# Kernel tuning notes

Measured on AMD Instinct MI355X. Metric: run time of the kernel, lower is better.

Reference implementation:

```python
import jax, jax.numpy as jnp
import numpy as np

B, N, D = 4, 2048, 512
H, HD = 8, 64  # heads, output_dim per head


def setup_inputs() -> dict:
    key = jax.random.key(0)
    ks = jax.random.split(key, 6)
    x = jax.random.normal(ks[0], (B, N, D), dtype=jnp.float32)
    adj = (jax.random.uniform(ks[1], (N, N)) < 0.1).astype(jnp.float32)
    adj = jnp.maximum(adj, jnp.eye(N, dtype=jnp.float32))
    s = 0.02
    Wq = jax.random.normal(ks[2], (D, H * HD), dtype=jnp.float32) * s
    Wk = jax.random.normal(ks[3], (D, H * HD), dtype=jnp.float32) * s
    Wv = jax.random.normal(ks[4], (D, H * HD), dtype=jnp.float32) * s
    bq = jnp.zeros((H * HD,), dtype=jnp.float32)
    bk = jnp.zeros((H * HD,), dtype=jnp.float32)
    bv = jnp.zeros((H * HD,), dtype=jnp.float32)
    return {"x": x, "adj": adj, "Wq": Wq, "bq": bq, "Wk": Wk, "bk": bk, "Wv": Wv, "bv": bv}


def reference(x, adj, Wq, bq, Wk, bk, Wv, bv):
    b, n, _ = x.shape
    q = (x @ Wq + bq).reshape(b, n, H, HD)
    k = (x @ Wk + bk).reshape(b, n, H, HD)
    v = (x @ Wv + bv).reshape(b, n, H, HD)
    # scores: [b, h, i, j]
    scores = jnp.einsum('bihd,bjhd->bhij', q, k) / jnp.sqrt(jnp.float32(HD))
    mask = jnp.where(adj == 0, jnp.float32(-1e9), jnp.float32(0.0))  # [n, n]
    scores = scores + mask[None, None, :, :]
    weights = jax.nn.softmax(scores, axis=-1)
    # dropout is identity at inference (training=False)
    out = jnp.einsum('bhij,bjhd->bihd', weights, v)
    return out.reshape(b, n, H * HD)
```

## Files before the change

### kernel.cpp

```cpp
#include <hip/hip_runtime.h>
#include <hip/hip_bf16.h>
#include <stdint.h>

#define NTOK 2048
#define DIN  512
#define QSCALE 0.18033688011112042f

typedef __attribute__((ext_vector_type(8))) short bf16x8;
typedef __attribute__((ext_vector_type(4))) short bf16x4;
typedef __attribute__((ext_vector_type(4))) float f32x4;

#define MFMA16(a, b, c) __builtin_amdgcn_mfma_f32_16x16x32_bf16((a), (b), (c), 0, 0, 0)

union u4bf8 { uint4 u; bf16x8 h; };

static __device__ __forceinline__ short f2bf(float f) {
  union { float f; uint32_t u; } v; v.f = f;
  uint32_t r = (v.u + 0x7FFFu + ((v.u >> 16) & 1u)) >> 16;
  return (short)r;
}

__global__ __launch_bounds__(256) void k_xbf(const float* __restrict__ x, short* __restrict__ xb) {
  size_t i = (size_t)blockIdx.x * 256 + threadIdx.x;
  const float4 v = *(const float4*)(x + i * 4);
  bf16x4 h;
  h[0] = f2bf(v.x); h[1] = f2bf(v.y); h[2] = f2bf(v.z); h[3] = f2bf(v.w);
  *(bf16x4*)(xb + i * 4) = h;
}

__global__ __launch_bounds__(256) void k_wt(const float* __restrict__ Wq,
                                            const float* __restrict__ Wk,
                                            const float* __restrict__ Wv,
                                            short* __restrict__ Wt) {
  const float* W = (blockIdx.z == 0) ? Wq : ((blockIdx.z == 1) ? Wk : Wv);
  short* Wo = Wt + (size_t)blockIdx.z * DIN * DIN;
  __shared__ float tile[32][33];
  int bo = blockIdx.x * 32, bc = blockIdx.y * 32;
  int tx = threadIdx.x & 31, ty = threadIdx.x >> 5;
#pragma unroll
  for (int q = 0; q < 4; ++q)
    tile[ty + q * 8][tx] = W[(bc + ty + q * 8) * DIN + bo + tx];
  __syncthreads();
#pragma unroll
  for (int q = 0; q < 4; ++q)
    Wo[(bo + ty + q * 8) * DIN + bc + tx] = f2bf(tile[tx][ty + q * 8]);
}

__global__ __launch_bounds__(256) void k_mask(const float* __restrict__ adj,
                                              unsigned long long* __restrict__ m64) {
  int wid = ((blockIdx.x * blockDim.x + threadIdx.x) >> 6);
  int lane = threadIdx.x & 63;
  int i = wid >> 5, wd = wid & 31;
  float a = adj[i * NTOK + wd * 64 + lane];
  unsigned long long b = __ballot(a != 0.0f);
  if (lane == 0) m64[i * 32 + wd] = b;
}

__global__ __launch_bounds__(256, 3) void k_qkv(const short* __restrict__ xb,
                                                const short* __restrict__ Wt,
                                                const float* __restrict__ bq,
                                                const float* __restrict__ bk,
                                                const float* __restrict__ bv,
                                                short* __restrict__ Qb, short* __restrict__ Kb,
                                                short* __restrict__ Vb) {
  __shared__ short As[2][128 * 40];
  __shared__ short Bs[2][128 * 40];
  const int z = blockIdx.z;
  const short* Wz = Wt + z * DIN * DIN;
  const float* bias = (z == 0) ? bq : ((z == 1) ? bk : bv);
  const int mbase = blockIdx.x * 128, nbase = blockIdx.y * 128;
  const int tid = threadIdx.x;
  const int lane = tid & 63, w = tid >> 6;
  const int wr = w >> 1, wc = w & 1;
  const int lrow = lane & 15, lgrp = lane >> 4;
  const int ra = tid >> 2, ca = tid & 3;

  f32x4 acc[4][4];
#pragma unroll
  for (int a = 0; a < 4; ++a)
#pragma unroll
    for (int b = 0; b < 4; ++b) acc[a][b] = (f32x4){0.f, 0.f, 0.f, 0.f};

  uint4 pA[2], pB[2];
#pragma unroll
  for (int u = 0; u < 2; ++u) {
    pA[u] = *(const uint4*)(xb + (size_t)(mbase + ra + u * 64) * DIN + ca * 8);
    pB[u] = *(const uint4*)(Wz + (size_t)(nbase + ra + u * 64) * DIN + ca * 8);
  }
#pragma unroll
  for (int u = 0; u < 2; ++u) {
    *(uint4*)(&As[0][(ra + u * 64) * 40 + ca * 8]) = pA[u];
    *(uint4*)(&Bs[0][(ra + u * 64) * 40 + ca * 8]) = pB[u];
  }
  __syncthreads();

  for (int t = 0; t < 16; ++t) {
    const int cur = t & 1, nxt = cur ^ 1;
    if (t < 15) {
      const int kb = (t + 1) * 32;
#pragma unroll
      for (int u = 0; u < 2; ++u) {
        pA[u] = *(const uint4*)(xb + (size_t)(mbase + ra + u * 64) * DIN + kb + ca * 8);
        pB[u] = *(const uint4*)(Wz + (size_t)(nbase + ra + u * 64) * DIN + kb + ca * 8);
      }
    }
    bf16x8 af[4], bf[4];
#pragma unroll
    for (int mi = 0; mi < 4; ++mi)
      af[mi] = *(bf16x8*)(&As[cur][(wr * 64 + mi * 16 + lrow) * 40 + lgrp * 8]);
#pragma unroll
    for (int ni = 0; ni < 4; ++ni)
      bf[ni] = *(bf16x8*)(&Bs[cur][(wc * 64 + ni * 16 + lrow) * 40 + lgrp * 8]);
#pragma unroll
    for (int mi = 0; mi < 4; ++mi)
#pragma unroll
      for (int ni = 0; ni < 4; ++ni) acc[mi][ni] = MFMA16(af[mi], bf[ni], acc[mi][ni]);

    if (t < 15) {
#pragma unroll
      for (int u = 0; u < 2; ++u) {
        *(uint4*)(&As[nxt][(ra + u * 64) * 40 + ca * 8]) = pA[u];
        *(uint4*)(&Bs[nxt][(ra + u * 64) * 40 + ca * 8]) = pB[u];
      }
      __syncthreads();
    }
  }

#pragma unroll
  for (int ni = 0; ni < 4; ++ni) {
    int go = nbase + wc * 64 + ni * 16 + lrow;
    float bv_ = bias[go];
    int h = go >> 6, d = go & 63;
#pragma unroll
    for (int mi = 0; mi < 4; ++mi) {
#pragma unroll
      for (int v = 0; v < 4; ++v) {
        int gm = mbase + wr * 64 + mi * 16 + lgrp * 4 + v;
        int b = gm >> 11, n = gm & 2047;
        int bh = b * 8 + h;
        float val = acc[mi][ni][v] + bv_;
        if (z == 0)
          Qb[(size_t)bh * (NTOK * 64) + n * 64 + d] = f2bf(val * QSCALE);
        else if (z == 1)
          Kb[(size_t)bh * (NTOK * 64) + n * 64 + d] = f2bf(val);
        else
          Vb[(size_t)bh * (64 * NTOK) + d * NTOK + n] = f2bf(val);
      }
    }
  }
}

__global__ __launch_bounds__(256, 3) void k_attn(const short* __restrict__ Qb,
                                                 const short* __restrict__ Kb,
                                                 const short* __restrict__ Vb,
                                                 const unsigned long long* __restrict__ m64,
                                                 float* __restrict__ out) {
  __shared__ char smem[36864];
  f32x4* ored = (f32x4*)smem;
  float* lsum = (float*)(smem + 16384);

  const int itile = blockIdx.x, bh = blockIdx.y;
  const int ibase = itile * 64;
  const int tid = threadIdx.x, lane = tid & 63, w = tid >> 6;
  const int wi = w >> 1, wj = w & 1;
  const int lrow = lane & 15, lgrp = lane >> 4;

  const short* Qp = Qb + (size_t)bh * (NTOK * 64);
  const short* Kp = Kb + (size_t)bh * (NTOK * 64);
  const short* Vp = Vb + (size_t)bh * (64 * NTOK);

  bf16x8 qa[2][2];
  const unsigned long long* mword[2];
#pragma unroll
  for (int ig = 0; ig < 2; ++ig) {
    const int qrow = ibase + wi * 32 + ig * 16 + lrow;
    qa[ig][0] = *(const bf16x8*)(Qp + (size_t)qrow * 64 + lgrp * 8);
    qa[ig][1] = *(const bf16x8*)(Qp + (size_t)qrow * 64 + 32 + lgrp * 8);
    mword[ig] = m64 + (size_t)qrow * 32;
  }

  const int r0 = tid >> 3, s0 = tid & 7;

  f32x4 oacc[2][4];
#pragma unroll
  for (int ig = 0; ig < 2; ++ig)
#pragma unroll
    for (int dn = 0; dn < 4; ++dn) oacc[ig][dn] = (f32x4){0.f, 0.f, 0.f, 0.f};
  float lrun[2] = {0.f, 0.f};

  uint4 pfK0 = *(const uint4*)(Kp + (size_t)r0 * 64 + s0 * 8);
  uint4 pfK1 = *(const uint4*)(Kp + (size_t)(r0 + 32) * 64 + s0 * 8);
  uint4 pfV0 = *(const uint4*)(Vp + (size_t)r0 * NTOK + s0 * 8);
  uint4 pfV1 = *(const uint4*)(Vp + (size_t)(r0 + 32) * NTOK + s0 * 8);
  unsigned long long mw[2] = {mword[0][0], mword[1][0]};
  {
    short* Kl0 = (short*)smem;
    short* Vl0 = (short*)(smem + 9216);
    *(uint4*)(Kl0 + r0 * 72 + s0 * 8) = pfK0;
    *(uint4*)(Kl0 + (r0 + 32) * 72 + s0 * 8) = pfK1;
    *(uint4*)(Vl0 + r0 * 72 + s0 * 8) = pfV0;
    *(uint4*)(Vl0 + (r0 + 32) * 72 + s0 * 8) = pfV1;
  }
  __syncthreads();

  for (int jt = 0; jt < 32; ++jt) {
    short* KlC = (short*)(smem + (jt & 1) * 18432);
    short* VlC = (short*)(smem + (jt & 1) * 18432 + 9216);
    unsigned long long mwn[2] = {0ull, 0ull};
    if (jt < 31) {
      const int jn = (jt + 1) * 64;
      pfK0 = *(const uint4*)(Kp + (size_t)(jn + r0) * 64 + s0 * 8);
      pfK1 = *(const uint4*)(Kp + (size_t)(jn + r0 + 32) * 64 + s0 * 8);
      pfV0 = *(const uint4*)(Vp + (size_t)r0 * NTOK + jn + s0 * 8);
      pfV1 = *(const uint4*)(Vp + (size_t)(r0 + 32) * NTOK + jn + s0 * 8);
      mwn[0] = mword[0][jt + 1];
      mwn[1] = mword[1][jt + 1];
    }

    uint32_t pk[2][2][2];
#pragma unroll
    for (int jsub = 0; jsub < 2; ++jsub) {
      const int krow = (wj * 32 + jsub * 16 + lrow) * 72;
      bf16x8 kf0 = *(bf16x8*)(KlC + krow + lgrp * 8);
      bf16x8 kf1 = *(bf16x8*)(KlC + krow + 32 + lgrp * 8);
#pragma unroll
      for (int ig = 0; ig < 2; ++ig) {
        f32x4 zz = (f32x4){0.f, 0.f, 0.f, 0.f};
        zz = MFMA16(kf0, qa[ig][0], zz);
        zz = MFMA16(kf1, qa[ig][1], zz);
        const uint32_t bits = (uint32_t)(mw[ig] >> (wj * 32 + jsub * 16 + lgrp * 4));
        float p0 = (bits & 1u) ? exp2f(zz[0]) : 0.f;
        float p1 = (bits & 2u) ? exp2f(zz[1]) : 0.f;
        float p2 = (bits & 4u) ? exp2f(zz[2]) : 0.f;
        float p3 = (bits & 8u) ? exp2f(zz[3]) : 0.f;
        lrun[ig] += (p0 + p1) + (p2 + p3);
        uint32_t w0, w1;
        asm("v_cvt_pk_bf16_f32 %0, %1, %2" : "=v"(w0) : "v"(p0), "v"(p1));
        asm("v_cvt_pk_bf16_f32 %0, %1, %2" : "=v"(w1) : "v"(p2), "v"(p3));
        pk[ig][jsub][0] = w0;
        pk[ig][jsub][1] = w1;
      }
    }

#pragma unroll
    for (int dn = 0; dn < 4; ++dn) {
      const int vrow = (dn * 16 + lrow) * 72 + wj * 32 + lgrp * 4;
      const uint2 v0 = *(const uint2*)(VlC + vrow);
      const uint2 v1 = *(const uint2*)(VlC + vrow + 16);
      u4bf8 vb;
      vb.u = (uint4){v0.x, v0.y, v1.x, v1.y};
#pragma unroll
      for (int ig = 0; ig < 2; ++ig) {
        u4bf8 pa;
        pa.u = (uint4){pk[ig][0][0], pk[ig][0][1], pk[ig][1][0], pk[ig][1][1]};
        oacc[ig][dn] = MFMA16(pa.h, vb.h, oacc[ig][dn]);
      }
    }

    if (jt < 31) {
      short* KlN = (short*)(smem + ((jt + 1) & 1) * 18432);
      short* VlN = (short*)(smem + ((jt + 1) & 1) * 18432 + 9216);
      *(uint4*)(KlN + r0 * 72 + s0 * 8) = pfK0;
      *(uint4*)(KlN + (r0 + 32) * 72 + s0 * 8) = pfK1;
      *(uint4*)(VlN + r0 * 72 + s0 * 8) = pfV0;
      *(uint4*)(VlN + (r0 + 32) * 72 + s0 * 8) = pfV1;
      mw[0] = mwn[0];
      mw[1] = mwn[1];
      __syncthreads();
    }
  }

  __syncthreads();

#pragma unroll
  for (int ig = 0; ig < 2; ++ig) {
    float s = lrun[ig];
    s += __shfl_xor(s, 16);
    s += __shfl_xor(s, 32);
    if (lane < 16) lsum[(w * 2 + ig) * 16 + lane] = s;
  }
  if (wj == 1) {
#pragma unroll
    for (int ig = 0; ig < 2; ++ig)
#pragma unroll
      for (int dn = 0; dn < 4; ++dn)
        ored[((wi * 2 + ig) * 4 + dn) * 64 + lane] = oacc[ig][dn];
  }
  __syncthreads();

  if (wj == 0) {
    const int b = bh >> 3, h = bh & 7;
#pragma unroll
    for (int ig = 0; ig < 2; ++ig) {
      const f32x4 la = *(const f32x4*)&lsum[((wi * 2 + 0) * 2 + ig) * 16 + lgrp * 4];
      const f32x4 lb = *(const f32x4*)&lsum[((wi * 2 + 1) * 2 + ig) * 16 + lgrp * 4];
      float inv[4];
#pragma unroll
      for (int v = 0; v < 4; ++v) inv[v] = 1.0f / (la[v] + lb[v]);
#pragma unroll
      for (int dn = 0; dn < 4; ++dn) {
        f32x4 s = oacc[ig][dn] + ored[((wi * 2 + ig) * 4 + dn) * 64 + lane];
#pragma unroll
        for (int v = 0; v < 4; ++v) {
          int i = ibase + wi * 32 + ig * 16 + lgrp * 4 + v;
          out[(size_t)(b * NTOK + i) * DIN + h * 64 + dn * 16 + lrow] = s[v] * inv[v];
        }
      }
    }
  }
}

extern "C" void kernel_launch(void* const* d_in, const int* in_sizes, int n_in,
                              void* d_out, int out_size, void* d_ws, size_t ws_size,
                              hipStream_t stream) {
  const float* x   = (const float*)d_in[0];
  const float* adj = (const float*)d_in[1];
  const float* Wq  = (const float*)d_in[2];
  const float* bq  = (const float*)d_in[3];
  const float* Wk  = (const float*)d_in[4];
  const float* bk  = (const float*)d_in[5];
  const float* Wv  = (const float*)d_in[6];
  const float* bv  = (const float*)d_in[7];
  float* out = (float*)d_out;

  char* ws = (char*)d_ws;
  short* Qb = (short*)(ws);
  short* Kb = (short*)(ws + (8u << 20));
  short* Vb = (short*)(ws + (16u << 20));
  short* Wt = (short*)(ws + (24u << 20));
  unsigned long long* m64 = (unsigned long long*)(ws + (26u << 20));
  short* xb = (short*)d_out;

  k_xbf<<<4096, 256, 0, stream>>>(x, xb);
  k_wt<<<dim3(16, 16, 3), 256, 0, stream>>>(Wq, Wk, Wv, Wt);
  k_mask<<<16384, 256, 0, stream>>>(adj, m64);
  k_qkv<<<dim3(64, 4, 3), 256, 0, stream>>>(xb, Wt, bq, bk, bv, Qb, Kb, Vb);
  k_attn<<<dim3(32, 32), 256, 0, stream>>>(Qb, Kb, Vb, m64, out);
}
```

Before: 120.7 us.

## Halve attention query tile to 32 rows and single-buffer K/V LDS

The attention kernel now processes 32 query rows per block instead of 64, doubling the grid to 64x32 blocks. K/V staging drops from double-buffered to single-buffered LDS, adding an extra barrier before each store, and launch bounds rise to 4 blocks per CU. The aim is higher occupancy and fewer per-thread registers, giving more blocks to fill the CUs. In exchange, each K/V tile is loaded from global memory twice as often, the extra barrier serialises load and compute, and MFMA work per LDS read is halved.

```diff
diff --git a/kernel.cpp b/kernel.cpp
--- a/kernel.cpp
+++ b/kernel.cpp
@@ -150,17 +150,19 @@
   }
 }
 
-__global__ __launch_bounds__(256, 3) void k_attn(const short* __restrict__ Qb,
+__global__ __launch_bounds__(256, 4) void k_attn(const short* __restrict__ Qb,
                                                  const short* __restrict__ Kb,
                                                  const short* __restrict__ Vb,
                                                  const unsigned long long* __restrict__ m64,
                                                  float* __restrict__ out) {
-  __shared__ char smem[36864];
+  __shared__ char smem[18432];
+  short* Kl = (short*)smem;
+  short* Vl = (short*)(smem + 9216);
   f32x4* ored = (f32x4*)smem;
-  float* lsum = (float*)(smem + 16384);
+  float* lsum = (float*)(smem + 8192);
 
   const int itile = blockIdx.x, bh = blockIdx.y;
-  const int ibase = itile * 64;
+  const int ibase = itile * 32;
   const int tid = threadIdx.x, lane = tid & 63, w = tid >> 6;
   const int wi = w >> 1, wj = w & 1;
   const int lrow = lane & 15, lgrp = lane >> 4;
@@ -169,142 +171,114 @@
   const short* Kp = Kb + (size_t)bh * (NTOK * 64);
   const short* Vp = Vb + (size_t)bh * (64 * NTOK);
 
-  bf16x8 qa[2][2];
-  const unsigned long long* mword[2];
-#pragma unroll
-  for (int ig = 0; ig < 2; ++ig) {
-    const int qrow = ibase + wi * 32 + ig * 16 + lrow;
-    qa[ig][0] = *(const bf16x8*)(Qp + (size_t)qrow * 64 + lgrp * 8);
-    qa[ig][1] = *(const bf16x8*)(Qp + (size_t)qrow * 64 + 32 + lgrp * 8);
-    mword[ig] = m64 + (size_t)qrow * 32;
-  }
+  const int qrow = ibase + wi * 16 + lrow;
+  bf16x8 qa[2];
+  qa[0] = *(const bf16x8*)(Qp + (size_t)qrow * 64 + lgrp * 8);
+  qa[1] = *(const bf16x8*)(Qp + (size_t)qrow * 64 + 32 + lgrp * 8);
+  const unsigned long long* mword = m64 + (size_t)qrow * 32;
 
   const int r0 = tid >> 3, s0 = tid & 7;
 
-  f32x4 oacc[2][4];
-#pragma unroll
-  for (int ig = 0; ig < 2; ++ig)
-#pragma unroll
-    for (int dn = 0; dn < 4; ++dn) oacc[ig][dn] = (f32x4){0.f, 0.f, 0.f, 0.f};
-  float lrun[2] = {0.f, 0.f};
+  f32x4 oacc[4];
+#pragma unroll
+  for (int dn = 0; dn < 4; ++dn) oacc[dn] = (f32x4){0.f, 0.f, 0.f, 0.f};
+  float lrun = 0.f;
 
   uint4 pfK0 = *(const uint4*)(Kp + (size_t)r0 * 64 + s0 * 8);
   uint4 pfK1 = *(const uint4*)(Kp + (size_t)(r0 + 32) * 64 + s0 * 8);
   uint4 pfV0 = *(const uint4*)(Vp + (size_t)r0 * NTOK + s0 * 8);
   uint4 pfV1 = *(const uint4*)(Vp + (size_t)(r0 + 32) * NTOK + s0 * 8);
-  unsigned long long mw[2] = {mword[0][0], mword[1][0]};
-  {
-    short* Kl0 = (short*)smem;
-    short* Vl0 = (short*)(smem + 9216);
-    *(uint4*)(Kl0 + r0 * 72 + s0 * 8) = pfK0;
-    *(uint4*)(Kl0 + (r0 + 32) * 72 + s0 * 8) = pfK1;
-    *(uint4*)(Vl0 + r0 * 72 + s0 * 8) = pfV0;
-    *(uint4*)(Vl0 + (r0 + 32) * 72 + s0 * 8) = pfV1;
-  }
+  unsigned long long mw = mword[0];
+  *(uint4*)(Kl + r0 * 72 + s0 * 8) = pfK0;
+  *(uint4*)(Kl + (r0 + 32) * 72 + s0 * 8) = pfK1;
+  *(uint4*)(Vl + r0 * 72 + s0 * 8) = pfV0;
+  *(uint4*)(Vl + (r0 + 32) * 72 + s0 * 8) = pfV1;
   __syncthreads();
 
   for (int jt = 0; jt < 32; ++jt) {
-    short* KlC = (short*)(smem + (jt & 1) * 18432);
-    short* VlC = (short*)(smem + (jt & 1) * 18432 + 9216);
-    unsigned long long mwn[2] = {0ull, 0ull};
+    unsigned long long mwn = 0ull;
     if (jt < 31) {
       const int jn = (jt + 1) * 64;
       pfK0 = *(const uint4*)(Kp + (size_t)(jn + r0) * 64 + s0 * 8);
       pfK1 = *(const uint4*)(Kp + (size_t)(jn + r0 + 32) * 64 + s0 * 8);
       pfV0 = *(const uint4*)(Vp + (size_t)r0 * NTOK + jn + s0 * 8);
       pfV1 = *(const uint4*)(Vp + (size_t)(r0 + 32) * NTOK + jn + s0 * 8);
-      mwn[0] = mword[0][jt + 1];
-      mwn[1] = mword[1][jt + 1];
-    }
-
-    uint32_t pk[2][2][2];
+      mwn = mword[jt + 1];
+    }
+
+    uint32_t pk[2][2];
 #pragma unroll
     for (int jsub = 0; jsub < 2; ++jsub) {
       const int krow = (wj * 32 + jsub * 16 + lrow) * 72;
-      bf16x8 kf0 = *(bf16x8*)(KlC + krow + lgrp * 8);
-      bf16x8 kf1 = *(bf16x8*)(KlC + krow + 32 + lgrp * 8);
-#pragma unroll
-      for (int ig = 0; ig < 2; ++ig) {
-        f32x4 zz = (f32x4){0.f, 0.f, 0.f, 0.f};
-        zz = MFMA16(kf0, qa[ig][0], zz);
-        zz = MFMA16(kf1, qa[ig][1], zz);
-        const uint32_t bits = (uint32_t)(mw[ig] >> (wj * 32 + jsub * 16 + lgrp * 4));
-        float p0 = (bits & 1u) ? exp2f(zz[0]) : 0.f;
-        float p1 = (bits & 2u) ? exp2f(zz[1]) : 0.f;
-        float p2 = (bits & 4u) ? exp2f(zz[2]) : 0.f;
-        float p3 = (bits & 8u) ? exp2f(zz[3]) : 0.f;
-        lrun[ig] += (p0 + p1) + (p2 + p3);
-        uint32_t w0, w1;
-        asm("v_cvt_pk_bf16_f32 %0, %1, %2" : "=v"(w0) : "v"(p0), "v"(p1));
-        asm("v_cvt_pk_bf16_f32 %0, %1, %2" : "=v"(w1) : "v"(p2), "v"(p3));
-        pk[ig][jsub][0] = w0;
-        pk[ig][jsub][1] = w1;
-      }
+      bf16x8 kf0 = *(bf16x8*)(Kl + krow + lgrp * 8);
+      bf16x8 kf1 = *(bf16x8*)(Kl + krow + 32 + lgrp * 8);
+      f32x4 zz = (f32x4){0.f, 0.f, 0.f, 0.f};
+      zz = MFMA16(kf0, qa[0], zz);
+      zz = MFMA16(kf1, qa[1], zz);
+      const uint32_t bits = (uint32_t)(mw >> (wj * 32 + jsub * 16 + lgrp * 4));
+      float p0 = (bits & 1u) ? exp2f(zz[0]) : 0.f;
+      float p1 = (bits & 2u) ? exp2f(zz[1]) : 0.f;
+      float p2 = (bits & 4u) ? exp2f(zz[2]) : 0.f;
+      float p3 = (bits & 8u) ? exp2f(zz[3]) : 0.f;
+      lrun += (p0 + p1) + (p2 + p3);
+      uint32_t w0, w1;
+      asm("v_cvt_pk_bf16_f32 %0, %1, %2" : "=v"(w0) : "v"(p0), "v"(p1));
+      asm("v_cvt_pk_bf16_f32 %0, %1, %2" : "=v"(w1) : "v"(p2), "v"(p3));
+      pk[jsub][0] = w0;
+      pk[jsub][1] = w1;
     }
 
 #pragma unroll
     for (int dn = 0; dn < 4; ++dn) {
       const int vrow = (dn * 16 + lrow) * 72 + wj * 32 + lgrp * 4;
-      const uint2 v0 = *(const uint2*)(VlC + vrow);
-      const uint2 v1 = *(const uint2*)(VlC + vrow + 16);
+      const uint2 v0 = *(const uint2*)(Vl + vrow);
+      const uint2 v1 = *(const uint2*)(Vl + vrow + 16);
       u4bf8 vb;
       vb.u = (uint4){v0.x, v0.y, v1.x, v1.y};
-#pragma unroll
-      for (int ig = 0; ig < 2; ++ig) {
-        u4bf8 pa;
-        pa.u = (uint4){pk[ig][0][0], pk[ig][0][1], pk[ig][1][0], pk[ig][1][1]};
-        oacc[ig][dn] = MFMA16(pa.h, vb.h, oacc[ig][dn]);
-      }
+      u4bf8 pa;
+      pa.u = (uint4){pk[0][0], pk[0][1], pk[1][0], pk[1][1]};
+      oacc[dn] = MFMA16(pa.h, vb.h, oacc[dn]);
     }
 
     if (jt < 31) {
-      short* KlN = (short*)(smem + ((jt + 1) & 1) * 18432);
-      short* VlN = (short*)(smem + ((jt + 1) & 1) * 18432 + 9216);
-      *(uint4*)(KlN + r0 * 72 + s0 * 8) = pfK0;
-      *(uint4*)(KlN + (r0 + 32) * 72 + s0 * 8) = pfK1;
-      *(uint4*)(VlN + r0 * 72 + s0 * 8) = pfV0;
-      *(uint4*)(VlN + (r0 + 32) * 72 + s0 * 8) = pfV1;
-      mw[0] = mwn[0];
-      mw[1] = mwn[1];
       __syncthreads();
-    }
-  }
-
-  __syncthreads();
-
-#pragma unroll
-  for (int ig = 0; ig < 2; ++ig) {
-    float s = lrun[ig];
+      *(uint4*)(Kl + r0 * 72 + s0 * 8) = pfK0;
+      *(uint4*)(Kl + (r0 + 32) * 72 + s0 * 8) = pfK1;
+      *(uint4*)(Vl + r0 * 72 + s0 * 8) = pfV0;
+      *(uint4*)(Vl + (r0 + 32) * 72 + s0 * 8) = pfV1;
+      mw = mwn;
+      __syncthreads();
+    }
+  }
+
+  __syncthreads();
+
+  {
+    float s = lrun;
     s += __shfl_xor(s, 16);
     s += __shfl_xor(s, 32);
-    if (lane < 16) lsum[(w * 2 + ig) * 16 + lane] = s;
+    if (lane < 16) lsum[(wi * 2 + wj) * 16 + lane] = s;
   }
   if (wj == 1) {
 #pragma unroll
-    for (int ig = 0; ig < 2; ++ig)
-#pragma unroll
-      for (int dn = 0; dn < 4; ++dn)
-        ored[((wi * 2 + ig) * 4 + dn) * 64 + lane] = oacc[ig][dn];
+    for (int dn = 0; dn < 4; ++dn) ored[(wi * 4 + dn) * 64 + lane] = oacc[dn];
   }
   __syncthreads();
 
   if (wj == 0) {
     const int b = bh >> 3, h = bh & 7;
-#pragma unroll
-    for (int ig = 0; ig < 2; ++ig) {
-      const f32x4 la = *(const f32x4*)&lsum[((wi * 2 + 0) * 2 + ig) * 16 + lgrp * 4];
-      const f32x4 lb = *(const f32x4*)&lsum[((wi * 2 + 1) * 2 + ig) * 16 + lgrp * 4];
-      float inv[4];
-#pragma unroll
-      for (int v = 0; v < 4; ++v) inv[v] = 1.0f / (la[v] + lb[v]);
-#pragma unroll
-      for (int dn = 0; dn < 4; ++dn) {
-        f32x4 s = oacc[ig][dn] + ored[((wi * 2 + ig) * 4 + dn) * 64 + lane];
-#pragma unroll
-        for (int v = 0; v < 4; ++v) {
-          int i = ibase + wi * 32 + ig * 16 + lgrp * 4 + v;
-          out[(size_t)(b * NTOK + i) * DIN + h * 64 + dn * 16 + lrow] = s[v] * inv[v];
-        }
+    const f32x4 la = *(const f32x4*)&lsum[(wi * 2 + 0) * 16 + lgrp * 4];
+    const f32x4 lb = *(const f32x4*)&lsum[(wi * 2 + 1) * 16 + lgrp * 4];
+    float inv[4];
+#pragma unroll
+    for (int v = 0; v < 4; ++v) inv[v] = 1.0f / (la[v] + lb[v]);
+#pragma unroll
+    for (int dn = 0; dn < 4; ++dn) {
+      f32x4 s = oacc[dn] + ored[(wi * 4 + dn) * 64 + lane];
+#pragma unroll
+      for (int v = 0; v < 4; ++v) {
+        int i = ibase + wi * 16 + lgrp * 4 + v;
+        out[(size_t)(b * NTOK + i) * DIN + h * 64 + dn * 16 + lrow] = s[v] * inv[v];
       }
     }
   }
@@ -335,5 +309,5 @@
   k_wt<<<dim3(16, 16, 3), 256, 0, stream>>>(Wq, Wk, Wv, Wt);
   k_mask<<<16384, 256, 0, stream>>>(adj, m64);
   k_qkv<<<dim3(64, 4, 3), 256, 0, stream>>>(xb, Wt, bq, bk, bv, Qb, Kb, Vb);
-  k_attn<<<dim3(32, 32), 256, 0, stream>>>(Qb, Kb, Vb, m64, out);
-}
+  k_attn<<<dim3(64, 32), 256, 0, stream>>>(Qb, Kb, Vb, m64, out);
+}
```

Result: slower. 124.2 us (+2.9%).
